# Performance work log

Measured on AMD Instinct MI355X. Metric: run time of the kernel, lower is better.

## Reference

```python
import jax, jax.numpy as jnp
import numpy as np

B, NV, L = 64, 8, 1024
P = 16            # patch_len == stride (non-overlapping)
D, H, DFF = 768, 12, 3072
K = D // H        # head dim 64
T = L // P        # 64 patches per sequence
N = B * NV        # 512 flattened sequences


def _ln(x, g, b, eps=1e-5):
    m = x.mean(-1, keepdims=True)
    v = x.var(-1, keepdims=True)
    return (x - m) / jnp.sqrt(v + eps) * g + b


def _pos_emb():
    pos = jnp.arange(T, dtype=jnp.float32)[:, None]
    div = jnp.exp(jnp.arange(0, D, 2, dtype=jnp.float32) * (-np.log(10000.0) / D))
    pe = jnp.zeros((T, D), jnp.float32)
    pe = pe.at[:, 0::2].set(jnp.sin(pos * div))
    pe = pe.at[:, 1::2].set(jnp.cos(pos * div))
    return pe


def setup_inputs() -> dict:
    key = jax.random.key(0)
    ks = jax.random.split(key, 24)
    rn = lambda k, s: jax.random.normal(k, s, jnp.float32) * 0.02
    return dict(
        x=jax.random.normal(ks[0], (B, NV, L), jnp.float32),
        W_patch=rn(ks[1], (P, D)), b_patch=jnp.zeros((D,), jnp.float32),
        ln1_g=jnp.ones((D,), jnp.float32), ln1_b=jnp.zeros((D,), jnp.float32),
        ln2_g=jnp.ones((D,), jnp.float32), ln2_b=jnp.zeros((D,), jnp.float32),
        mu_r=jax.random.uniform(ks[2], (D,), jnp.float32),
        mu_w=jax.random.uniform(ks[3], (D,), jnp.float32),
        mu_k=jax.random.uniform(ks[4], (D,), jnp.float32),
        mu_v=jax.random.uniform(ks[5], (D,), jnp.float32),
        mu_a=jax.random.uniform(ks[6], (D,), jnp.float32),
        mu_g=jax.random.uniform(ks[7], (D,), jnp.float32),
        mu_c=jax.random.uniform(ks[8], (D,), jnp.float32),
        Wr=rn(ks[9], (D, D)), Wk=rn(ks[10], (D, D)), Wv=rn(ks[11], (D, D)),
        Wg=rn(ks[12], (D, D)), Ww=rn(ks[13], (D, D)), w0=rn(ks[14], (D,)),
        Wa=rn(ks[15], (D, D)), a0=jnp.zeros((D,), jnp.float32),
        Wo=rn(ks[16], (D, D)),
        gn_g=jnp.ones((D,), jnp.float32), gn_b=jnp.zeros((D,), jnp.float32),
        Wc1=rn(ks[17], (D, DFF)), Wc2=rn(ks[18], (DFF, D)),
        W_proj=rn(ks[19], (D, P)), b_proj=jnp.zeros((P,), jnp.float32),
    )


def reference(x, W_patch, b_patch, ln1_g, ln1_b, ln2_g, ln2_b,
              mu_r, mu_w, mu_k, mu_v, mu_a, mu_g, mu_c,
              Wr, Wk, Wv, Wg, Ww, w0, Wa, a0, Wo, gn_g, gn_b,
              Wc1, Wc2, W_proj, b_proj):
    # --- patch embedding (stride == patch_len -> plain reshape) ---
    patches = x.reshape(B, NV, T, P).reshape(N, T, P)
    h = patches @ W_patch + b_patch + _pos_emb()        # [N, T, D]

    # --- RWKV7 time mixing ---
    xx = _ln(h, ln1_g, ln1_b)
    sh = jnp.pad(xx[:, :-1], ((0, 0), (1, 0), (0, 0)))  # token shift
    lerp = lambda mu: xx + (sh - xx) * mu
    r = (lerp(mu_r) @ Wr).reshape(N, T, H, K)
    k = (lerp(mu_k) @ Wk).reshape(N, T, H, K)
    v = (lerp(mu_v) @ Wv).reshape(N, T, H, K)
    w = jnp.exp(-jnp.exp(lerp(mu_w) @ Ww + w0)).reshape(N, T, H, K)  # decay in (0,1)
    a = jax.nn.sigmoid(lerp(mu_a) @ Wa + a0).reshape(N, T, H, K)     # in-context lr
    g = jax.nn.sigmoid(lerp(mu_g) @ Wg)                              # output gate [N,T,D]
    kk = k / (jnp.linalg.norm(k, axis=-1, keepdims=True) + 1e-6)     # removal key

    seq = tuple(jnp.transpose(t, (1, 0, 2, 3)) for t in (r, w, k, v, kk, a))

    def step(S, inp):
        # S: [N, H, V, K] value-by-key state (generalized delta rule)
        r_t, w_t, k_t, v_t, kk_t, a_t = inp
        S = S * w_t[:, :, None, :]
        sa = jnp.einsum('nhvk,nhk->nhv', S, kk_t)
        S = S - jnp.einsum('nhv,nhk->nhvk', sa, kk_t * a_t) \
              + jnp.einsum('nhv,nhk->nhvk', v_t, k_t)
        y = jnp.einsum('nhvk,nhk->nhv', S, r_t)
        return S, y

    S0 = jnp.zeros((N, H, K, K), x.dtype)
    _, ys = jax.lax.scan(step, S0, seq)
    y = jnp.transpose(ys, (1, 0, 2, 3))                 # [N, T, H, K]

    # per-head group norm (RWKV7 uses eps = 64e-5)
    m = y.mean(-1, keepdims=True)
    var = y.var(-1, keepdims=True)
    y = (y - m) / jnp.sqrt(var + 64e-5)
    y = y.reshape(N, T, D) * gn_g + gn_b
    h = h + (y * g) @ Wo

    # --- channel mixing (squared-ReLU FFN) ---
    xc = _ln(h, ln2_g, ln2_b)
    shc = jnp.pad(xc[:, :-1], ((0, 0), (1, 0), (0, 0)))
    xk = xc + (shc - xc) * mu_c
    h = h + jnp.square(jax.nn.relu(xk @ Wc1)) @ Wc2

    # --- projection back to patch space ---
    return h @ W_proj + b_proj                          # [N, T, P]
```

## Files before the change

### kernel.cpp

```cpp
#include <hip/hip_runtime.h>
#include <hip/hip_bf16.h>
#include <math.h>

typedef unsigned short u16;
typedef unsigned int u32;
typedef _Float16 f16x8 __attribute__((ext_vector_type(8)));
typedef float f32x4 __attribute__((ext_vector_type(4)));

#define DEV static __device__ __forceinline__

constexpr int D = 768;
constexpr int HH = 12;
constexpr int KD = 64;
constexpr int T = 64;
constexpr int NSEQ = 512;
constexpr int MROWS = NSEQ * T;
constexpr int DFF = 3072;
constexpr int PP = 16;

DEV u16 f2h(float f){ union{_Float16 h; u16 u;} c; c.h = (_Float16)f; return c.u; }
DEV float h2f(u16 u){ union{u16 u; _Float16 h;} c; c.u = u; return (float)c.h; }
DEV void gld_lds16(const u16* g, u16* l){
  __builtin_amdgcn_global_load_lds((const __attribute__((address_space(1))) void*)g,
                                   (__attribute__((address_space(3))) void*)l, 16, 0, 0);
}
DEV int lsw(int row, int kgrp){ return row * 32 + ((((row >> 2) ^ row) & 3) ^ kgrp) * 8; }

struct TpArgs { const float* src[7]; u16* dst[7]; };
__global__ __launch_bounds__(256) void k_transpose7(TpArgs a){
  __shared__ float tile[32][33];
  int z = blockIdx.z;
  const float* W = a.src[z];
  u16* WT = a.dst[z];
  int c0 = blockIdx.x * 32, r0 = blockIdx.y * 32;
  int tx = threadIdx.x, ty = threadIdx.y;
  #pragma unroll
  for (int i = 0; i < 32; i += 8)
    tile[ty + i][tx] = W[(size_t)(r0 + ty + i) * D + (c0 + tx)];
  __syncthreads();
  #pragma unroll
  for (int i = 0; i < 32; i += 8)
    WT[(size_t)(c0 + ty + i) * D + (r0 + tx)] = f2h(tile[tx][ty + i]);
}

__global__ __launch_bounds__(256) void k_transpose(const float* __restrict__ W, u16* __restrict__ WT,
                                                   int R, int C){
  __shared__ float tile[32][33];
  int c0 = blockIdx.x * 32, r0 = blockIdx.y * 32;
  int tx = threadIdx.x, ty = threadIdx.y;
  #pragma unroll
  for (int i = 0; i < 32; i += 8)
    tile[ty + i][tx] = W[(size_t)(r0 + ty + i) * C + (c0 + tx)];
  __syncthreads();
  #pragma unroll
  for (int i = 0; i < 32; i += 8)
    WT[(size_t)(c0 + ty + i) * R + (r0 + tx)] = f2h(tile[tx][ty + i]);
}

__global__ void k_pe(float* __restrict__ pe){
  int idx = blockIdx.x * 256 + threadIdx.x;
  if (idx >= T * D) return;
  int t = idx / D, d = idx % D;
  float dv = __expf((float)(d & ~1) * (-9.210340371976184f / (float)D));
  float ang = (float)t * dv;
  pe[idx] = (d & 1) ? cosf(ang) : sinf(ang);
}

struct MuArgs { const float* mu[6]; };
__global__ __launch_bounds__(256) void k_mu16(MuArgs a, u16* __restrict__ mu16){
  int z = blockIdx.x;
  #pragma unroll
  for (int j = 0; j < 3; j++){
    int d = threadIdx.x + j * 256;
    mu16[z * D + d] = f2h(a.mu[z][d]);
  }
}

__global__ __launch_bounds__(256) void k_patch_ln(const float* __restrict__ x, const float* __restrict__ Wp,
                                                  const float* __restrict__ bp, const float* __restrict__ pe,
                                                  const float* __restrict__ g, const float* __restrict__ b,
                                                  float* __restrict__ h, u16* __restrict__ xx16){
  int lane = threadIdx.x & 63;
  int row = blockIdx.x * 4 + (threadIdx.x >> 6);
  int t = row & (T - 1);
  const float* xr = x + (size_t)row * PP;
  float xs[PP];
  #pragma unroll
  for (int p = 0; p < PP; p++) xs[p] = xr[p];
  float v[12], s = 0.f, sq = 0.f;
  #pragma unroll
  for (int j = 0; j < 12; j++){
    int d = lane + j * 64;
    float acc = bp[d] + pe[t * D + d];
    #pragma unroll
    for (int p = 0; p < PP; p++) acc = fmaf(xs[p], Wp[p * D + d], acc);
    v[j] = acc; s += acc; sq = fmaf(acc, acc, sq);
  }
  #pragma unroll
  for (int o = 32; o; o >>= 1){ s += __shfl_xor(s, o); sq += __shfl_xor(sq, o); }
  float mean = s * (1.f / 768.f);
  float rstd = rsqrtf(sq * (1.f / 768.f) - mean * mean + 1e-5f);
  float* hrow = h + (size_t)row * D;
  u16* xrow = xx16 + (size_t)row * D;
  #pragma unroll
  for (int j = 0; j < 12; j++){
    int d = lane + j * 64;
    hrow[d] = v[j];
    xrow[d] = f2h((v[j] - mean) * rstd * g[d] + b[d]);
  }
}

__global__ __launch_bounds__(256) void k_ln2(const float* __restrict__ X, const float* __restrict__ g,
                                             const float* __restrict__ b, const float* __restrict__ mu,
                                             u16* __restrict__ out){
  int lane = threadIdx.x & 63;
  int row = blockIdx.x * 4 + (threadIdx.x >> 6);
  int t = row & (T - 1);
  const float* xr = X + (size_t)row * D;
  float v[12], s = 0.f, sq = 0.f;
  #pragma unroll
  for (int j = 0; j < 12; j++){ v[j] = xr[lane + j * 64]; s += v[j]; sq += v[j] * v[j]; }
  #pragma unroll
  for (int o = 32; o; o >>= 1){ s += __shfl_xor(s, o); sq += __shfl_xor(sq, o); }
  float mean = s * (1.f / 768.f);
  float rstd = rsqrtf(sq * (1.f / 768.f) - mean * mean + 1e-5f);
  float p[12], meanp = 0.f, rstdp = 0.f;
  if (t){
    const float* xp = xr - D;
    float sp = 0.f, sqp = 0.f;
    #pragma unroll
    for (int j = 0; j < 12; j++){ p[j] = xp[lane + j * 64]; sp += p[j]; sqp += p[j] * p[j]; }
    #pragma unroll
    for (int o = 32; o; o >>= 1){ sp += __shfl_xor(sp, o); sqp += __shfl_xor(sqp, o); }
    meanp = sp * (1.f / 768.f);
    rstdp = rsqrtf(sqp * (1.f / 768.f) - meanp * meanp + 1e-5f);
  }
  u16* orow = out + (size_t)row * D;
  #pragma unroll
  for (int j = 0; j < 12; j++){
    int d = lane + j * 64;
    float cm = (v[j] - mean) * rstd * g[d] + b[d];
    float cp = t ? (p[j] - meanp) * rstdp * g[d] + b[d] : 0.f;
    orow[d] = f2h(cm + (cp - cm) * mu[d]);
  }
}

template<int ACT>
__global__ __launch_bounds__(256) void k_g16(const u16* __restrict__ A, const u16* __restrict__ BT,
                                             u16* __restrict__ outH, float* __restrict__ outF,
                                             int Kd, int Nc){
  __shared__ __align__(16) u16 As[2][128 * 32];
  __shared__ __align__(16) u16 Bs[2][128 * 32];
  int tid = threadIdx.x;
  int m0 = blockIdx.x * 128, n0 = blockIdx.y * 128;
  int wv = tid >> 6, lane = tid & 63;
  int wr = (wv >> 1) * 64, wc = (wv & 1) * 64;
  int lr = lane & 15, kgrp = lane >> 4;
  int r0 = wv * 16 + (lane >> 2);
  int cbg = ((((r0 >> 2) ^ r0) & 3) ^ (lane & 3)) * 8;
  const u16* sA0 = A + (size_t)(m0 + r0) * Kd + cbg;
  const u16* sA1 = A + (size_t)(m0 + r0 + 64) * Kd + cbg;
  const u16* sB0 = BT + (size_t)(n0 + r0) * Kd + cbg;
  const u16* sB1 = BT + (size_t)(n0 + r0 + 64) * Kd + cbg;
  int cb = (lane & 3) * 8;
  int o0 = r0 * 32 + cb, o1 = (r0 + 64) * 32 + cb;
  f32x4 acc[4][4] = {};
  int NT = Kd >> 5;

  gld_lds16(sA0, &As[0][o0]);
  gld_lds16(sA1, &As[0][o1]);
  gld_lds16(sB0, &Bs[0][o0]);
  gld_lds16(sB1, &Bs[0][o1]);
  __syncthreads();
  int cur = 0;
  for (int kt = 0; kt < NT; kt++){
    if (kt + 1 < NT){
      int k0 = (kt + 1) << 5;
      gld_lds16(sA0 + k0, &As[cur ^ 1][o0]);
      gld_lds16(sA1 + k0, &As[cur ^ 1][o1]);
      gld_lds16(sB0 + k0, &Bs[cur ^ 1][o0]);
      gld_lds16(sB1 + k0, &Bs[cur ^ 1][o1]);
    }
    f16x8 af[4], bf[4];
    #pragma unroll
    for (int mi = 0; mi < 4; mi++) af[mi] = *(const f16x8*)&As[cur][lsw(wr + mi * 16 + lr, kgrp)];
    #pragma unroll
    for (int ni = 0; ni < 4; ni++) bf[ni] = *(const f16x8*)&Bs[cur][lsw(wc + ni * 16 + lr, kgrp)];
    #pragma unroll
    for (int mi = 0; mi < 4; mi++){
      #pragma unroll
      for (int ni = 0; ni < 4; ni++){
        acc[mi][ni] = __builtin_amdgcn_mfma_f32_16x16x32_f16(af[mi], bf[ni], acc[mi][ni], 0, 0, 0);
      }
    }
    __syncthreads();
    cur ^= 1;
  }

  int rowb = m0 + wr + (lane >> 4) * 4;
  int colb = n0 + wc + lr;
  #pragma unroll
  for (int mi = 0; mi < 4; mi++){
    #pragma unroll
    for (int ni = 0; ni < 4; ni++){
      int gcol = colb + ni * 16;
      #pragma unroll
      for (int i = 0; i < 4; i++){
        int grow = rowb + mi * 16 + i;
        float xv = acc[mi][ni][i];
        size_t o = (size_t)grow * Nc + gcol;
        if (ACT == 3){ float rl = fmaxf(xv, 0.f); outH[o] = f2h(rl * rl); }
        else outF[o] += xv;
      }
    }
  }
}

struct MixArgs {
  const u16* b[6]; const float* bias[6]; const u16* mu16;
  u16* outh[6]; int act[6];
};
__global__ __launch_bounds__(256) void k_mix_lerp(const u16* __restrict__ X16, MixArgs args, int Kd, int Nc){
  __shared__ __align__(16) u16 As[2][128 * 32];
  __shared__ __align__(16) u16 Bs[2][128 * 32];
  int tid = threadIdx.x, z = blockIdx.z;
  const u16* BT = args.b[z];
  const u16* mu16 = args.mu16 + z * D;
  int m0 = blockIdx.x * 128, n0 = blockIdx.y * 128;
  int wv = tid >> 6, lane = tid & 63;
  int wr = (wv >> 1) * 64, wc = (wv & 1) * 64;
  int lr = lane & 15, kgrp = lane >> 4;
  int r0 = wv * 16 + (lane >> 2);
  int cbg = ((((r0 >> 2) ^ r0) & 3) ^ (lane & 3)) * 8;
  const u16* sB0 = BT + (size_t)(n0 + r0) * Kd + cbg;
  const u16* sB1 = BT + (size_t)(n0 + r0 + 64) * Kd + cbg;
  int cb = (lane & 3) * 8;
  int o0 = r0 * 32 + cb, o1 = (r0 + 64) * 32 + cb;
  int rr0 = tid >> 2, cg0 = tid & 3;
  int rr1 = (256 + tid) >> 2, cg1 = (256 + tid) & 3;
  bool tz0 = ((m0 + rr0) & (T - 1)) != 0;
  bool tz1 = ((m0 + rr1) & (T - 1)) != 0;
  const u16* srcA0 = X16 + (size_t)(m0 + rr0) * Kd + cg0 * 8;
  const u16* srcA1 = X16 + (size_t)(m0 + rr1) * Kd + cg1 * 8;
  int wsl0 = lsw(rr0, cg0), wsl1 = lsw(rr1, cg1);
  f32x4 acc[4][4] = {};
  int NT = Kd >> 5;

  gld_lds16(sB0, &Bs[0][o0]);
  gld_lds16(sB1, &Bs[0][o1]);
  {
    f16x8 c0 = *(const f16x8*)srcA0;
    f16x8 m0v = *(const f16x8*)(mu16 + cg0 * 8);
    f16x8 p0 = {};
    if (tz0) p0 = *(const f16x8*)(srcA0 - Kd);
    *(f16x8*)&As[0][wsl0] = c0 + (p0 - c0) * m0v;
    f16x8 c1 = *(const f16x8*)srcA1;
    f16x8 m1v = *(const f16x8*)(mu16 + cg1 * 8);
    f16x8 p1 = {};
    if (tz1) p1 = *(const f16x8*)(srcA1 - Kd);
    *(f16x8*)&As[0][wsl1] = c1 + (p1 - c1) * m1v;
  }
  __syncthreads();
  int cur = 0;
  for (int kt = 0; kt < NT; kt++){
    bool hn = (kt + 1 < NT);
    f16x8 nc0, np0, nm0, nc1, np1, nm1;
    if (hn){
      int k0 = (kt + 1) << 5;
      gld_lds16(sB0 + k0, &Bs[cur ^ 1][o0]);
      gld_lds16(sB1 + k0, &Bs[cur ^ 1][o1]);
      nc0 = *(const f16x8*)(srcA0 + k0);
      nm0 = *(const f16x8*)(mu16 + k0 + cg0 * 8);
      np0 = f16x8{};
      if (tz0) np0 = *(const f16x8*)(srcA0 + k0 - Kd);
      nc1 = *(const f16x8*)(srcA1 + k0);
      nm1 = *(const f16x8*)(mu16 + k0 + cg1 * 8);
      np1 = f16x8{};
      if (tz1) np1 = *(const f16x8*)(srcA1 + k0 - Kd);
    }
    f16x8 af[4], bf[4];
    #pragma unroll
    for (int mi = 0; mi < 4; mi++) af[mi] = *(const f16x8*)&As[cur][lsw(wr + mi * 16 + lr, kgrp)];
    #pragma unroll
    for (int ni = 0; ni < 4; ni++) bf[ni] = *(const f16x8*)&Bs[cur][lsw(wc + ni * 16 + lr, kgrp)];
    #pragma unroll
    for (int mi = 0; mi < 4; mi++){
      #pragma unroll
      for (int ni = 0; ni < 4; ni++){
        acc[mi][ni] = __builtin_amdgcn_mfma_f32_16x16x32_f16(af[mi], bf[ni], acc[mi][ni], 0, 0, 0);
      }
    }
    if (hn){
      *(f16x8*)&As[cur ^ 1][wsl0] = nc0 + (np0 - nc0) * nm0;
      *(f16x8*)&As[cur ^ 1][wsl1] = nc1 + (np1 - nc1) * nm1;
    }
    __syncthreads();
    cur ^= 1;
  }

  int act = args.act[z];
  const float* bias = args.bias[z];
  u16* outh = args.outh[z];
  int rowb = m0 + wr + (lane >> 4) * 4;
  int colb = n0 + wc + lr;
  #pragma unroll
  for (int mi = 0; mi < 4; mi++){
    #pragma unroll
    for (int ni = 0; ni < 4; ni++){
      int gcol = colb + ni * 16;
      float bv = bias ? bias[gcol] : 0.f;
      #pragma unroll
      for (int i = 0; i < 4; i++){
        int grow = rowb + mi * 16 + i;
        float xv = acc[mi][ni][i] + bv;
        size_t o = (size_t)grow * Nc + gcol;
        if (act == 2) xv = 1.f / (1.f + __expf(-xv));
        outh[o] = f2h(xv);
      }
    }
  }
}

constexpr int TS = 8;
__global__ __launch_bounds__(256) void k_rwkv(const u16* __restrict__ rb16, const u16* __restrict__ wp16,
                                              const u16* __restrict__ kb16, const u16* __restrict__ vb,
                                              const u16* __restrict__ ab, const u16* __restrict__ gbuf,
                                              const float* __restrict__ gng, const float* __restrict__ gnb,
                                              u16* __restrict__ yg){
  __shared__ __align__(16) float ls_w[TS][64], ls_k[TS][64], ls_r[TS][64];
  __shared__ float ls_v[TS][64];
  __shared__ float ls_kk[TS][64], ls_ka[TS][64];
  __shared__ float sa_red[2][4][64];
  __shared__ float y_red[2][4][64];
  int nh = blockIdx.x;
  int n = nh / HH, hh = nh - n * HH;
  int tid = threadIdx.x;
  int wv = __builtin_amdgcn_readfirstlane(tid >> 6);
  int lane = tid & 63;
  float S[16];
  #pragma unroll
  for (int i = 0; i < 16; i++) S[i] = 0.f;
  int dcol = hh * KD + lane;
  float gscale = gng[dcol], gshift = gnb[dcol];
  size_t hbase = (size_t)n * T * D + hh * KD;
  int jbase = wv * 16;
  int strow = tid >> 5;
  int stcol = (tid & 31) * 2;
  for (int tt = 0; tt < T; tt += TS){
    __syncthreads();
    size_t gofs = hbase + (size_t)(tt + strow) * D + stcol;
    u32 w2 = *(const u32*)(wp16 + gofs);
    u32 k2 = *(const u32*)(kb16 + gofs);
    u32 r2 = *(const u32*)(rb16 + gofs);
    u32 v2 = *(const u32*)(vb + gofs);
    u32 a2 = *(const u32*)(ab + gofs);
    float k0 = h2f((u16)(k2 & 0xffffu));
    float k1 = h2f((u16)(k2 >> 16));
    float ss = fmaf(k0, k0, k1 * k1);
    #pragma unroll
    for (int o = 16; o; o >>= 1) ss += __shfl_xor(ss, o);
    float inv = 1.f / (sqrtf(ss) + 1e-6f);
    float kk0 = k0 * inv, kk1 = k1 * inv;
    ls_w[strow][stcol]     = __expf(-__expf(h2f((u16)(w2 & 0xffffu))));
    ls_w[strow][stcol + 1] = __expf(-__expf(h2f((u16)(w2 >> 16))));
    ls_k[strow][stcol]     = k0;
    ls_k[strow][stcol + 1] = k1;
    ls_r[strow][stcol]     = h2f((u16)(r2 & 0xffffu));
    ls_r[strow][stcol + 1] = h2f((u16)(r2 >> 16));
    ls_v[strow][stcol]     = h2f((u16)(v2 & 0xffffu));
    ls_v[strow][stcol + 1] = h2f((u16)(v2 >> 16));
    ls_kk[strow][stcol]     = kk0;
    ls_kk[strow][stcol + 1] = kk1;
    ls_ka[strow][stcol]     = kk0 * h2f((u16)(a2 & 0xffffu));
    ls_ka[strow][stcol + 1] = kk1 * h2f((u16)(a2 >> 16));
    __syncthreads();
    for (int s = 0; s < TS; s++){
      int sg = tt + s;
      int pb = sg & 1;
      f32x4 W4[4], KK4[4];
      #pragma unroll
      for (int q = 0; q < 4; q++){
        W4[q]  = *(const f32x4*)&ls_w[s][jbase + q * 4];
        KK4[q] = *(const f32x4*)&ls_kk[s][jbase + q * 4];
      }
      float sap = 0.f;
      #pragma unroll
      for (int q = 0; q < 4; q++){
        #pragma unroll
        for (int i = 0; i < 4; i++){
          S[q * 4 + i] *= W4[q][i];
          sap += S[q * 4 + i] * KK4[q][i];
        }
      }
      sa_red[pb][wv][lane] = sap;
      __syncthreads();
      if (wv == 0 && sg > 0){
        int pp = pb ^ 1;
        float y = y_red[pp][0][lane] + y_red[pp][1][lane] + y_red[pp][2][lane] + y_red[pp][3][lane];
        float s1 = y, s2 = y * y;
        #pragma unroll
        for (int o = 32; o; o >>= 1){ s1 += __shfl_xor(s1, o); s2 += __shfl_xor(s2, o); }
        float mean = s1 * (1.f / 64.f);
        float var = s2 * (1.f / 64.f) - mean * mean;
        float yn = (y - mean) * rsqrtf(var + 64e-5f);
        size_t pidx = hbase + (size_t)(sg - 1) * D + lane;
        float gv = h2f(gbuf[pidx]);
        yg[pidx] = f2h((yn * gscale + gshift) * gv);
      }
      float sa = sa_red[pb][0][lane] + sa_red[pb][1][lane] + sa_red[pb][2][lane] + sa_red[pb][3][lane];
      float nsa = -sa;
      float vl = ls_v[s][lane];
      f32x4 K4[4], KA4[4], R4[4];
      #pragma unroll
      for (int q = 0; q < 4; q++){
        K4[q]  = *(const f32x4*)&ls_k[s][jbase + q * 4];
        KA4[q] = *(const f32x4*)&ls_ka[s][jbase + q * 4];
        R4[q]  = *(const f32x4*)&ls_r[s][jbase + q * 4];
      }
      float yp = 0.f;
      #pragma unroll
      for (int q = 0; q < 4; q++){
        #pragma unroll
        for (int i = 0; i < 4; i++){
          S[q * 4 + i] = fmaf(vl, K4[q][i], S[q * 4 + i]);
          S[q * 4 + i] = fmaf(nsa, KA4[q][i], S[q * 4 + i]);
          yp += S[q * 4 + i] * R4[q][i];
        }
      }
      y_red[pb][wv][lane] = yp;
    }
  }
  __syncthreads();
  if (wv == 0){
    int pp = (T - 1) & 1;
    float y = y_red[pp][0][lane] + y_red[pp][1][lane] + y_red[pp][2][lane] + y_red[pp][3][lane];
    float s1 = y, s2 = y * y;
    #pragma unroll
    for (int o = 32; o; o >>= 1){ s1 += __shfl_xor(s1, o); s2 += __shfl_xor(s2, o); }
    float mean = s1 * (1.f / 64.f);
    float var = s2 * (1.f / 64.f) - mean * mean;
    float yn = (y - mean) * rsqrtf(var + 64e-5f);
    size_t pidx = hbase + (size_t)(T - 1) * D + lane;
    float gv = h2f(gbuf[pidx]);
    yg[pidx] = f2h((yn * gscale + gshift) * gv);
  }
}

__global__ __launch_bounds__(256) void k_proj(const float* __restrict__ Hb, const float* __restrict__ Wp,
                                              const float* __restrict__ bp, float* __restrict__ out){
  int lane = threadIdx.x & 63;
  int row = blockIdx.x * 4 + (threadIdx.x >> 6);
  int p = lane & 15, q = lane >> 4;
  const float* hr = Hb + (size_t)row * D;
  float acc = 0.f;
  #pragma unroll 8
  for (int i = 0; i < 192; i++){
    int d = q * 192 + i;
    acc = fmaf(hr[d], Wp[d * PP + p], acc);
  }
  acc += __shfl_xor(acc, 16);
  acc += __shfl_xor(acc, 32);
  if (q == 0) out[(size_t)row * PP + p] = acc + bp[p];
}

extern "C" void kernel_launch(void* const* d_in, const int* in_sizes, int n_in,
                              void* d_out, int out_size, void* d_ws, size_t ws_size,
                              hipStream_t stream){
  (void)in_sizes; (void)n_in; (void)out_size;
  const float* x       = (const float*)d_in[0];
  const float* W_patch = (const float*)d_in[1];
  const float* b_patch = (const float*)d_in[2];
  const float* ln1_g   = (const float*)d_in[3];
  const float* ln1_b   = (const float*)d_in[4];
  const float* ln2_g   = (const float*)d_in[5];
  const float* ln2_b   = (const float*)d_in[6];
  const float* mu_r    = (const float*)d_in[7];
  const float* mu_w    = (const float*)d_in[8];
  const float* mu_k    = (const float*)d_in[9];
  const float* mu_v    = (const float*)d_in[10];
  const float* mu_a    = (const float*)d_in[11];
  const float* mu_g    = (const float*)d_in[12];
  const float* mu_c    = (const float*)d_in[13];
  const float* Wr      = (const float*)d_in[14];
  const float* Wk      = (const float*)d_in[15];
  const float* Wv      = (const float*)d_in[16];
  const float* Wg      = (const float*)d_in[17];
  const float* Ww      = (const float*)d_in[18];
  const float* w0      = (const float*)d_in[19];
  const float* Wa      = (const float*)d_in[20];
  const float* a0      = (const float*)d_in[21];
  const float* Wo      = (const float*)d_in[22];
  const float* gn_g    = (const float*)d_in[23];
  const float* gn_b    = (const float*)d_in[24];
  const float* Wc1     = (const float*)d_in[25];
  const float* Wc2     = (const float*)d_in[26];
  const float* W_proj  = (const float*)d_in[27];
  const float* b_proj  = (const float*)d_in[28];
  float* out = (float*)d_out;

  char* ws = (char*)d_ws;
  size_t off = 0;
  auto alloc = [&](size_t bytes) -> char* {
    char* p = ws + off;
    off = (off + bytes + 255) & ~(size_t)255;
    return p;
  };

  const size_t WB = (size_t)D * D * 2;
  u16* WrT  = (u16*)alloc(WB);
  u16* WwT  = (u16*)alloc(WB);
  u16* WkT  = (u16*)alloc(WB);
  u16* WvT  = (u16*)alloc(WB);
  u16* WaT  = (u16*)alloc(WB);
  u16* WgT  = (u16*)alloc(WB);
  u16* WoT  = (u16*)alloc(WB);
  u16* Wc1T = (u16*)alloc((size_t)D * DFF * 2);
  u16* Wc2T = (u16*)alloc((size_t)DFF * D * 2);
  float* pe = (float*)alloc((size_t)T * D * 4);
  u16* mu16 = (u16*)alloc((size_t)6 * D * 2);
  size_t wend = off;

  int nch = 1;
  size_t Mc = MROWS;
  while (nch < 128){
    size_t need = wend + Mc * 13824 + 64 * 256;
    if (need <= ws_size) break;
    nch *= 2;
    Mc >>= 1;
  }
  float* hbuf = (float*)alloc(Mc * 768 * 4);
  u16* xx     = (u16*)alloc(Mc * 768 * 2);
  u16* wp     = (u16*)alloc(Mc * 768 * 2);
  u16* rb     = (u16*)alloc(Mc * 768 * 2);
  u16* kb     = (u16*)alloc(Mc * 768 * 2);
  u16* vb     = (u16*)alloc(Mc * 768 * 2);
  u16* ab     = (u16*)alloc(Mc * 768 * 2);
  u16* gb     = (u16*)alloc(Mc * 768 * 2);
  u16* ygb = ab;
  u16* mid = xx;
  u16* xkb = gb;

  dim3 tb(32, 8);
  TpArgs ta;
  ta.src[0] = Wr; ta.dst[0] = WrT;
  ta.src[1] = Ww; ta.dst[1] = WwT;
  ta.src[2] = Wk; ta.dst[2] = WkT;
  ta.src[3] = Wv; ta.dst[3] = WvT;
  ta.src[4] = Wa; ta.dst[4] = WaT;
  ta.src[5] = Wg; ta.dst[5] = WgT;
  ta.src[6] = Wo; ta.dst[6] = WoT;
  k_transpose7<<<dim3(24, 24, 7), tb, 0, stream>>>(ta);
  k_transpose<<<dim3(96, 24), tb, 0, stream>>>(Wc1, Wc1T, D, DFF);
  k_transpose<<<dim3(24, 96), tb, 0, stream>>>(Wc2, Wc2T, DFF, D);
  k_pe<<<dim3(192), dim3(256), 0, stream>>>(pe);
  MuArgs ma;
  ma.mu[0] = mu_r; ma.mu[1] = mu_w; ma.mu[2] = mu_k;
  ma.mu[3] = mu_v; ma.mu[4] = mu_a; ma.mu[5] = mu_g;
  k_mu16<<<dim3(6), dim3(256), 0, stream>>>(ma, mu16);

  MixArgs margs;
  const u16* wts[6] = {WrT, WwT, WkT, WvT, WaT, WgT};
  const float* bss[6] = {nullptr, w0, nullptr, nullptr, a0, nullptr};
  u16* oh[6] = {rb, wp, kb, vb, ab, gb};
  int acts[6] = {0, 1, 0, 0, 2, 2};
  margs.mu16 = mu16;
  for (int z = 0; z < 6; z++){
    margs.b[z] = wts[z];
    margs.bias[z] = bss[z];
    margs.outh[z] = oh[z];
    margs.act[z] = acts[z];
  }

  for (int c = 0; c < nch; ++c){
    const float* xc = x + (size_t)c * Mc * PP;
    float* outc = out + (size_t)c * Mc * PP;
    int mcb = (int)(Mc / 128);

    k_patch_ln<<<dim3((int)(Mc / 4)), dim3(256), 0, stream>>>(xc, W_patch, b_patch, pe, ln1_g, ln1_b, hbuf, xx);

    k_mix_lerp<<<dim3(mcb, 6, 6), 256, 0, stream>>>(xx, margs, D, D);

    k_rwkv<<<dim3((int)(Mc / T) * HH), dim3(256), 0, stream>>>(rb, wp, kb, vb, ab, gb, gn_g, gn_b, ygb);

    k_g16<4><<<dim3(mcb, 6), 256, 0, stream>>>(ygb, WoT, nullptr, hbuf, D, D);

    k_ln2<<<dim3((int)(Mc / 4)), dim3(256), 0, stream>>>(hbuf, ln2_g, ln2_b, mu_c, xkb);
    k_g16<3><<<dim3(mcb, DFF / 128), 256, 0, stream>>>(xkb, Wc1T, mid, nullptr, D, DFF);
    k_g16<4><<<dim3(mcb, 6), 256, 0, stream>>>(mid, Wc2T, nullptr, hbuf, DFF, D);

    k_proj<<<dim3((int)(Mc / 4)), dim3(256), 0, stream>>>(hbuf, W_proj, b_proj, outc);
  }
}
```

Before: 1.608 ms.

## Process two heads per RWKV block with two waves per head

Result: faster. 1.566 ms (-2.6%).

```diff
diff --git a/kernel.cpp b/kernel.cpp
--- a/kernel.cpp
+++ b/kernel.cpp
@@ -327,76 +327,79 @@
                                               const u16* __restrict__ ab, const u16* __restrict__ gbuf,
                                               const float* __restrict__ gng, const float* __restrict__ gnb,
                                               u16* __restrict__ yg){
-  __shared__ __align__(16) float ls_w[TS][64], ls_k[TS][64], ls_r[TS][64];
-  __shared__ float ls_v[TS][64];
-  __shared__ float ls_kk[TS][64], ls_ka[TS][64];
-  __shared__ float sa_red[2][4][64];
-  __shared__ float y_red[2][4][64];
-  int nh = blockIdx.x;
-  int n = nh / HH, hh = nh - n * HH;
+  __shared__ __align__(16) float ls_w[2][TS][64], ls_k[2][TS][64], ls_r[2][TS][64];
+  __shared__ float ls_v[2][TS][64];
+  __shared__ float ls_kk[2][TS][64], ls_ka[2][TS][64];
+  __shared__ float sa_red[2][2][2][64];
+  __shared__ float y_red[2][2][2][64];
+  int nh2 = blockIdx.x;
+  constexpr int HP = HH / 2;
+  int n = nh2 / HP, hp = nh2 - n * HP;
+  int hh0 = hp * 2;
   int tid = threadIdx.x;
   int wv = __builtin_amdgcn_readfirstlane(tid >> 6);
   int lane = tid & 63;
-  float S[16];
-  #pragma unroll
-  for (int i = 0; i < 16; i++) S[i] = 0.f;
-  int dcol = hh * KD + lane;
+  int hd = wv >> 1, wh = wv & 1;
+  float S[32];
+  #pragma unroll
+  for (int i = 0; i < 32; i++) S[i] = 0.f;
+  int dcol = (hh0 + hd) * KD + lane;
   float gscale = gng[dcol], gshift = gnb[dcol];
-  size_t hbase = (size_t)n * T * D + hh * KD;
-  int jbase = wv * 16;
+  size_t hbaseA = (size_t)n * T * D + (size_t)hh0 * KD;
+  size_t hbase = hbaseA + (size_t)hd * KD;
+  int jbase = wh * 32;
   int strow = tid >> 5;
   int stcol = (tid & 31) * 2;
   for (int tt = 0; tt < T; tt += TS){
     __syncthreads();
-    size_t gofs = hbase + (size_t)(tt + strow) * D + stcol;
-    u32 w2 = *(const u32*)(wp16 + gofs);
-    u32 k2 = *(const u32*)(kb16 + gofs);
-    u32 r2 = *(const u32*)(rb16 + gofs);
-    u32 v2 = *(const u32*)(vb + gofs);
-    u32 a2 = *(const u32*)(ab + gofs);
-    float k0 = h2f((u16)(k2 & 0xffffu));
-    float k1 = h2f((u16)(k2 >> 16));
-    float ss = fmaf(k0, k0, k1 * k1);
-    #pragma unroll
-    for (int o = 16; o; o >>= 1) ss += __shfl_xor(ss, o);
-    float inv = 1.f / (sqrtf(ss) + 1e-6f);
-    float kk0 = k0 * inv, kk1 = k1 * inv;
-    ls_w[strow][stcol]     = __expf(-__expf(h2f((u16)(w2 & 0xffffu))));
-    ls_w[strow][stcol + 1] = __expf(-__expf(h2f((u16)(w2 >> 16))));
-    ls_k[strow][stcol]     = k0;
-    ls_k[strow][stcol + 1] = k1;
-    ls_r[strow][stcol]     = h2f((u16)(r2 & 0xffffu));
-    ls_r[strow][stcol + 1] = h2f((u16)(r2 >> 16));
-    ls_v[strow][stcol]     = h2f((u16)(v2 & 0xffffu));
-    ls_v[strow][stcol + 1] = h2f((u16)(v2 >> 16));
-    ls_kk[strow][stcol]     = kk0;
-    ls_kk[strow][stcol + 1] = kk1;
-    ls_ka[strow][stcol]     = kk0 * h2f((u16)(a2 & 0xffffu));
-    ls_ka[strow][stcol + 1] = kk1 * h2f((u16)(a2 >> 16));
+    #pragma unroll
+    for (int h2 = 0; h2 < 2; h2++){
+      size_t gofs = hbaseA + (size_t)h2 * KD + (size_t)(tt + strow) * D + stcol;
+      u32 w2 = *(const u32*)(wp16 + gofs);
+      u32 k2 = *(const u32*)(kb16 + gofs);
+      u32 r2 = *(const u32*)(rb16 + gofs);
+      u32 v2 = *(const u32*)(vb + gofs);
+      u32 a2 = *(const u32*)(ab + gofs);
+      float k0 = h2f((u16)(k2 & 0xffffu));
+      float k1 = h2f((u16)(k2 >> 16));
+      float ss = fmaf(k0, k0, k1 * k1);
+      #pragma unroll
+      for (int o = 16; o; o >>= 1) ss += __shfl_xor(ss, o);
+      float inv = 1.f / (sqrtf(ss) + 1e-6f);
+      float kk0 = k0 * inv, kk1 = k1 * inv;
+      ls_w[h2][strow][stcol]     = __expf(-__expf(h2f((u16)(w2 & 0xffffu))));
+      ls_w[h2][strow][stcol + 1] = __expf(-__expf(h2f((u16)(w2 >> 16))));
+      ls_k[h2][strow][stcol]     = k0;
+      ls_k[h2][strow][stcol + 1] = k1;
+      ls_r[h2][strow][stcol]     = h2f((u16)(r2 & 0xffffu));
+      ls_r[h2][strow][stcol + 1] = h2f((u16)(r2 >> 16));
+      ls_v[h2][strow][stcol]     = h2f((u16)(v2 & 0xffffu));
+      ls_v[h2][strow][stcol + 1] = h2f((u16)(v2 >> 16));
+      ls_kk[h2][strow][stcol]     = kk0;
+      ls_kk[h2][strow][stcol + 1] = kk1;
+      ls_ka[h2][strow][stcol]     = kk0 * h2f((u16)(a2 & 0xffffu));
+      ls_ka[h2][strow][stcol + 1] = kk1 * h2f((u16)(a2 >> 16));
+    }
     __syncthreads();
     for (int s = 0; s < TS; s++){
       int sg = tt + s;
       int pb = sg & 1;
-      f32x4 W4[4], KK4[4];
-      #pragma unroll
-      for (int q = 0; q < 4; q++){
-        W4[q]  = *(const f32x4*)&ls_w[s][jbase + q * 4];
-        KK4[q] = *(const f32x4*)&ls_kk[s][jbase + q * 4];
-      }
       float sap = 0.f;
       #pragma unroll
-      for (int q = 0; q < 4; q++){
+      for (int q = 0; q < 8; q++){
+        f32x4 W4  = *(const f32x4*)&ls_w[hd][s][jbase + q * 4];
+        f32x4 KK4 = *(const f32x4*)&ls_kk[hd][s][jbase + q * 4];
         #pragma unroll
         for (int i = 0; i < 4; i++){
-          S[q * 4 + i] *= W4[q][i];
-          sap += S[q * 4 + i] * KK4[q][i];
+          S[q * 4 + i] *= W4[i];
+          sap += S[q * 4 + i] * KK4[i];
         }
       }
-      sa_red[pb][wv][lane] = sap;
+      sa_red[pb][hd][wh][lane] = sap;
       __syncthreads();
-      if (wv == 0 && sg > 0){
+      if (wh == 0 && sg > 0){
         int pp = pb ^ 1;
-        float y = y_red[pp][0][lane] + y_red[pp][1][lane] + y_red[pp][2][lane] + y_red[pp][3][lane];
+        float y = y_red[pp][hd][0][lane] + y_red[pp][hd][1][lane];
         float s1 = y, s2 = y * y;
         #pragma unroll
         for (int o = 32; o; o >>= 1){ s1 += __shfl_xor(s1, o); s2 += __shfl_xor(s2, o); }
@@ -407,33 +410,29 @@
         float gv = h2f(gbuf[pidx]);
         yg[pidx] = f2h((yn * gscale + gshift) * gv);
       }
-      float sa = sa_red[pb][0][lane] + sa_red[pb][1][lane] + sa_red[pb][2][lane] + sa_red[pb][3][lane];
+      float sa = sa_red[pb][hd][0][lane] + sa_red[pb][hd][1][lane];
       float nsa = -sa;
-      float vl = ls_v[s][lane];
-      f32x4 K4[4], KA4[4], R4[4];
-      #pragma unroll
-      for (int q = 0; q < 4; q++){
-        K4[q]  = *(const f32x4*)&ls_k[s][jbase + q * 4];
-        KA4[q] = *(const f32x4*)&ls_ka[s][jbase + q * 4];
-        R4[q]  = *(const f32x4*)&ls_r[s][jbase + q * 4];
-      }
+      float vl = ls_v[hd][s][lane];
       float yp = 0.f;
       #pragma unroll
-      for (int q = 0; q < 4; q++){
+      for (int q = 0; q < 8; q++){
+        f32x4 K4  = *(const f32x4*)&ls_k[hd][s][jbase + q * 4];
+        f32x4 KA4 = *(const f32x4*)&ls_ka[hd][s][jbase + q * 4];
+        f32x4 R4  = *(const f32x4*)&ls_r[hd][s][jbase + q * 4];
         #pragma unroll
         for (int i = 0; i < 4; i++){
-          S[q * 4 + i] = fmaf(vl, K4[q][i], S[q * 4 + i]);
-          S[q * 4 + i] = fmaf(nsa, KA4[q][i], S[q * 4 + i]);
-          yp += S[q * 4 + i] * R4[q][i];
+          S[q * 4 + i] = fmaf(vl, K4[i], S[q * 4 + i]);
+          S[q * 4 + i] = fmaf(nsa, KA4[i], S[q * 4 + i]);
+          yp += S[q * 4 + i] * R4[i];
         }
       }
-      y_red[pb][wv][lane] = yp;
+      y_red[pb][hd][wh][lane] = yp;
     }
   }
   __syncthreads();
-  if (wv == 0){
+  if (wh == 0){
     int pp = (T - 1) & 1;
-    float y = y_red[pp][0][lane] + y_red[pp][1][lane] + y_red[pp][2][lane] + y_red[pp][3][lane];
+    float y = y_red[pp][hd][0][lane] + y_red[pp][hd][1][lane];
     float s1 = y, s2 = y * y;
     #pragma unroll
     for (int o = 32; o; o >>= 1){ s1 += __shfl_xor(s1, o); s2 += __shfl_xor(s2, o); }
@@ -580,7 +579,7 @@
 
     k_mix_lerp<<<dim3(mcb, 6, 6), 256, 0, stream>>>(xx, margs, D, D);
 
-    k_rwkv<<<dim3((int)(Mc / T) * HH), dim3(256), 0, stream>>>(rb, wp, kb, vb, ab, gb, gn_g, gn_b, ygb);
+    k_rwkv<<<dim3((int)(Mc / T) * (HH / 2)), dim3(256), 0, stream>>>(rb, wp, kb, vb, ab, gb, gn_g, gn_b, ygb);
 
     k_g16<4><<<dim3(mcb, 6), 256, 0, stream>>>(ygb, WoT, nullptr, hbuf, D, D);
 
```
